# Optimization experiments

Measured on AMD Instinct MI355X. Metric: run time of the kernel, lower is better.

The kernel has to match this reference:

```python
import jax, jax.numpy as jnp
import numpy as np

B, H, W, C = 4, 224, 224, 256
HEADS = 8
WIN = 7
N = WIN * WIN  # 49 tokens per window
MLP_HID = 4 * C
EPS = 1e-5


def _rel_index(w):
    coords = np.stack(np.meshgrid(np.arange(w), np.arange(w), indexing='ij'))  # (2,w,w)
    cf = coords.reshape(2, -1)                       # (2, w*w)
    rc = cf[:, :, None] - cf[:, None, :]             # (2, N, N)
    rc = rc.transpose(1, 2, 0).astype(np.int64)      # (N, N, 2)
    rc[:, :, 0] += w - 1
    rc[:, :, 1] += w - 1
    rc[:, :, 0] *= 2 * w - 1
    return jnp.asarray(rc.sum(-1), dtype=jnp.int32)  # (N, N)


def setup_inputs() -> dict:
    key = jax.random.key(0)
    ks = jax.random.split(key, 6)
    std = 0.02
    return {
        'x': jax.random.normal(ks[0], (B, H, W, C), dtype=jnp.float32),
        'norm1_g': jnp.ones((C,), jnp.float32),
        'norm1_b': jnp.zeros((C,), jnp.float32),
        'qkv_w': jax.random.normal(ks[1], (3 * C, C), jnp.float32) * std,
        'qkv_b': jnp.zeros((3 * C,), jnp.float32),
        'bias_table': jax.random.normal(ks[2], ((2 * WIN - 1) ** 2, HEADS), jnp.float32) * std,
        'proj_w': jax.random.normal(ks[3], (C, C), jnp.float32) * std,
        'proj_b': jnp.zeros((C,), jnp.float32),
        'norm2_g': jnp.ones((C,), jnp.float32),
        'norm2_b': jnp.zeros((C,), jnp.float32),
        'fc1_w': jax.random.normal(ks[4], (MLP_HID, C), jnp.float32) * std,
        'fc1_b': jnp.zeros((MLP_HID,), jnp.float32),
        'fc2_w': jax.random.normal(ks[5], (C, MLP_HID), jnp.float32) * std,
        'fc2_b': jnp.zeros((C,), jnp.float32),
        'rel_index': _rel_index(WIN),
    }


def _layernorm(x, g, b):
    mu = jnp.mean(x, axis=-1, keepdims=True)
    var = jnp.mean(jnp.square(x - mu), axis=-1, keepdims=True)
    return (x - mu) * jax.lax.rsqrt(var + EPS) * g + b


def reference(x, norm1_g, norm1_b, qkv_w, qkv_b, bias_table, proj_w, proj_b,
              norm2_g, norm2_b, fc1_w, fc1_b, fc2_w, fc2_b, rel_index):
    Bc, Hc, Wc, Cc = x.shape
    d = Cc // HEADS
    scale = d ** -0.5
    nh, nw = Hc // WIN, Wc // WIN

    shortcut = x
    h = _layernorm(x, norm1_g, norm1_b)

    # window_partition: (B,H,W,C) -> (B*nW, N, C)
    wins = h.reshape(Bc, nh, WIN, nw, WIN, Cc).transpose(0, 1, 3, 2, 4, 5)
    wins = wins.reshape(-1, N, Cc)

    # qkv projection and split into heads
    qkv = wins @ qkv_w.T + qkv_b                                  # (Bw, N, 3C)
    qkv = qkv.reshape(-1, N, 3, HEADS, d).transpose(2, 0, 3, 1, 4)  # (3, Bw, h, N, d)
    q, k, v = qkv[0], qkv[1], qkv[2]

    attn = jnp.einsum('bhnd,bhmd->bhnm', q, k) * scale            # (Bw, h, N, N)
    bias = bias_table[rel_index.reshape(-1)].reshape(N, N, HEADS).transpose(2, 0, 1)
    attn = jax.nn.softmax(attn + bias[None], axis=-1)

    o = jnp.einsum('bhnm,bhmd->bhnd', attn, v)                    # (Bw, h, N, d)
    o = o.transpose(0, 2, 1, 3).reshape(-1, N, Cc)
    o = o @ proj_w.T + proj_b

    # window_reverse: (B*nW, N, C) -> (B,H,W,C)
    o = o.reshape(Bc, nh, nw, WIN, WIN, Cc).transpose(0, 1, 3, 2, 4, 5)
    o = o.reshape(Bc, Hc, Wc, Cc)

    x = shortcut + o
    h2 = _layernorm(x, norm2_g, norm2_b)
    m = jax.nn.gelu(h2 @ fc1_w.T + fc1_b, approximate=False) @ fc2_w.T + fc2_b
    return x + m
```

## Files before the change

### kernel.cpp

```cpp
#include <hip/hip_runtime.h>

typedef unsigned short u16;
typedef __bf16 bf16x8 __attribute__((ext_vector_type(8)));
typedef float f32x4 __attribute__((ext_vector_type(4)));

#define TOKENS 200704
#define QK_ELEMS 51380224UL

__device__ __forceinline__ u16 f2b(float f) {
    __bf16 h = (__bf16)f;
    return __builtin_bit_cast(u16, h);
}

#define GLDS(g, l) __builtin_amdgcn_global_load_lds( \
    (const __attribute__((address_space(1))) void*)(g), \
    (__attribute__((address_space(3))) void*)(l), 16, 0, 0)

#define MFMA __builtin_amdgcn_mfma_f32_16x16x32_bf16

template<int EPI>
__global__ __launch_bounds__(512, 2)
void gemm256(const u16* __restrict__ A, const u16* __restrict__ W,
             const float* __restrict__ bias, int nt, int K, long moff,
             u16* __restrict__ outb, float* __restrict__ outf,
             const float* __restrict__ res,
             const float* __restrict__ g2, const float* __restrict__ b2,
             u16* __restrict__ h2o)
{
    __shared__ u16 As[2][256 * 64];
    __shared__ u16 Bs[2][256 * 64];
    const int tid  = threadIdx.x;
    const int wave = tid >> 6, lane = tid & 63;

    const int nwg = gridDim.x, bidO = blockIdx.x;
    const int qq = nwg >> 3, rr = nwg & 7;
    const int xcd = bidO & 7, idxx = bidO >> 3;
    const int bid = (xcd < rr) ? (xcd * (qq + 1) + idxx)
                               : (rr * (qq + 1) + (xcd - rr) * qq + idxx);

    const int bm = bid / nt, bn = bid % nt;
    const long m0 = (long)bm * 256;
    const int  n0 = bn * 256;
    const int wr = wave >> 2, wc = wave & 3;
    const int lr = lane & 15, lg = lane >> 4;
    const int crow   = lane >> 3;
    const int ccol_s = ((lane & 7) ^ crow) * 8;
    const int swz    = (lr & 7) * 8;

    f32x4 acc[8][4] = {};

    auto stage = [&](int buf, int k0) {
#pragma unroll
        for (int p = 0; p < 4; ++p) {
            const int i = p * 8 + wave;
            const int row = i * 8 + crow;
            GLDS(A + (m0 + row) * (long)K + k0 + ccol_s, &As[buf][i * 512]);
            GLDS(W + (long)(n0 + row) * K + k0 + ccol_s, &Bs[buf][i * 512]);
        }
    };

    auto compute = [&](int buf) {
        bf16x8 bfr[2][4];
#pragma unroll
        for (int kk2 = 0; kk2 < 2; ++kk2)
#pragma unroll
            for (int fn = 0; fn < 4; ++fn)
                bfr[kk2][fn] = *reinterpret_cast<const bf16x8*>(
                    &Bs[buf][(wc * 64 + fn * 16 + lr) * 64 + ((kk2 * 32 + lg * 8) ^ swz)]);
        bf16x8 aq[2][2], an[2][2];
#pragma unroll
        for (int p = 0; p < 2; ++p)
#pragma unroll
            for (int kk2 = 0; kk2 < 2; ++kk2)
                aq[p][kk2] = *reinterpret_cast<const bf16x8*>(
                    &As[buf][(wr * 128 + p * 16 + lr) * 64 + ((kk2 * 32 + lg * 8) ^ swz)]);
#pragma unroll
        for (int q = 0; q < 4; ++q) {
            bf16x8 (&cur)[2][2] = (q & 1) ? an : aq;
            bf16x8 (&nxt)[2][2] = (q & 1) ? aq : an;
            if (q < 3) {
#pragma unroll
                for (int p = 0; p < 2; ++p)
#pragma unroll
                    for (int kk2 = 0; kk2 < 2; ++kk2)
                        nxt[p][kk2] = *reinterpret_cast<const bf16x8*>(
                            &As[buf][(wr * 128 + (2 * (q + 1) + p) * 16 + lr) * 64 + ((kk2 * 32 + lg * 8) ^ swz)]);
            }
            __builtin_amdgcn_s_setprio(1);
#pragma unroll
            for (int p = 0; p < 2; ++p)
#pragma unroll
                for (int kk2 = 0; kk2 < 2; ++kk2)
#pragma unroll
                    for (int fn = 0; fn < 4; ++fn)
                        acc[2 * q + p][fn] = MFMA(cur[p][kk2], bfr[kk2][fn], acc[2 * q + p][fn], 0, 0, 0);
            __builtin_amdgcn_s_setprio(0);
        }
    };

    const int nk = K >> 6;
    stage(0, 0);
    stage(1, 64);
    int k = 128;
    for (int t = 0; t < nk - 1; ++t) {
        asm volatile("s_waitcnt vmcnt(8)" ::: "memory");
        __builtin_amdgcn_s_barrier();
        __builtin_amdgcn_sched_barrier(0);
        compute(t & 1);
        __builtin_amdgcn_s_barrier();
        __builtin_amdgcn_sched_barrier(0);
        if (t + 2 < nk) {
            stage(t & 1, k); k += 64;
            __builtin_amdgcn_sched_barrier(0);
        }
    }
    asm volatile("s_waitcnt vmcnt(0)" ::: "memory");
    __builtin_amdgcn_s_barrier();
    __builtin_amdgcn_sched_barrier(0);
    compute((nk - 1) & 1);

    if constexpr (EPI == 1) {
        __shared__ float red[2][256][4];
        float g2c[4], b2c[4];
#pragma unroll
        for (int fn = 0; fn < 4; ++fn) {
            const int n = wc * 64 + fn * 16 + lr;
            g2c[fn] = g2[n]; b2c[fn] = b2[n];
        }
#pragma unroll
        for (int fm = 0; fm < 8; ++fm) {
#pragma unroll
            for (int r = 0; r < 4; ++r) {
                const long m = m0 + wr * 128 + fm * 16 + lg * 4 + r;
                float s = 0.f, s2 = 0.f;
#pragma unroll
                for (int fn = 0; fn < 4; ++fn) {
                    const int n = wc * 64 + fn * 16 + lr;
                    const float x2 = acc[fm][fn][r] + bias[n] + res[m * 256 + n];
                    acc[fm][fn][r] = x2;
                    outf[m * 256 + n] = x2;
                    s += x2; s2 += x2 * x2;
                }
#pragma unroll
                for (int d = 1; d < 16; d <<= 1) { s += __shfl_xor(s, d); s2 += __shfl_xor(s2, d); }
                if (lr == 0) {
                    const int tok = wr * 128 + fm * 16 + lg * 4 + r;
                    red[0][tok][wc] = s; red[1][tok][wc] = s2;
                }
            }
        }
        __syncthreads();
#pragma unroll
        for (int fm = 0; fm < 8; ++fm) {
#pragma unroll
            for (int r = 0; r < 4; ++r) {
                const int tok = wr * 128 + fm * 16 + lg * 4 + r;
                const float s  = red[0][tok][0] + red[0][tok][1] + red[0][tok][2] + red[0][tok][3];
                const float q  = red[1][tok][0] + red[1][tok][1] + red[1][tok][2] + red[1][tok][3];
                const float mu = s * 0.00390625f;
                const float rs = rsqrtf(q * 0.00390625f - mu * mu + 1e-5f);
                const long m = m0 + tok;
#pragma unroll
                for (int fn = 0; fn < 4; ++fn) {
                    const int n = wc * 64 + fn * 16 + lr;
                    h2o[m * 256 + n] = f2b((acc[fm][fn][r] - mu) * rs * g2c[fn] + b2c[fn]);
                }
            }
        }
    } else {
#pragma unroll
        for (int fm = 0; fm < 8; ++fm) {
#pragma unroll
            for (int r = 0; r < 4; ++r) {
                const long m = m0 + wr * 128 + fm * 16 + lg * 4 + r;
                size_t mpart = 0;
                if (EPI == 0) {
                    const int gm = (int)(m + moff);
                    const int b = gm / 50176;
                    const int rem = gm % 50176;
                    const int y = rem / 224, x = rem % 224;
                    const int win = (b * 32 + y / 7) * 32 + x / 7;
                    const int pos = (y % 7) * 7 + (x % 7);
                    mpart = (size_t)win * 12544 + (size_t)pos * 32;
                }
#pragma unroll
                for (int fn = 0; fn < 4; ++fn) {
                    const int n = n0 + wc * 64 + fn * 16 + lr;
                    const float v = acc[fm][fn][r];
                    if (EPI == 0) {
                        const int sec = n >> 8, hd = (n >> 5) & 7, d = n & 31;
                        const float sc = (sec == 0) ? 0.17677669529663687f : 1.0f;
                        outb[sec * QK_ELEMS + mpart + hd * 1568 + d] = f2b((v + bias[n]) * sc);
                    } else if (EPI == 2) {
                        const float t = v + bias[n];
                        const float s = t * (1.5957691216f + 0.07135481627f * t * t);
                        const float g = t * __builtin_amdgcn_rcpf(1.0f + __expf(-s));
                        outb[m * 1024 + n] = f2b(g);
                    } else {
                        outf[m * 256 + n] += v + bias[n];
                    }
                }
            }
        }
    }
}

__global__ __launch_bounds__(256)
void layernorm_k(const float* __restrict__ in, const float* __restrict__ g,
                 const float* __restrict__ bb, u16* __restrict__ out)
{
    const int token = blockIdx.x * 4 + (threadIdx.x >> 6);
    const int lane = threadIdx.x & 63;
    const float4 v = *reinterpret_cast<const float4*>(in + (size_t)token * 256 + lane * 4);
    float s  = v.x + v.y + v.z + v.w;
    float s2 = v.x * v.x + v.y * v.y + v.z * v.z + v.w * v.w;
#pragma unroll
    for (int m = 1; m < 64; m <<= 1) { s += __shfl_xor(s, m); s2 += __shfl_xor(s2, m); }
    const float mu  = s * (1.0f / 256.0f);
    const float var = s2 * (1.0f / 256.0f) - mu * mu;
    const float rs  = rsqrtf(var + 1e-5f);
    const float4 gv = *reinterpret_cast<const float4*>(g + lane * 4);
    const float4 bv = *reinterpret_cast<const float4*>(bb + lane * 4);
    ushort4 o;
    o.x = f2b((v.x - mu) * rs * gv.x + bv.x);
    o.y = f2b((v.y - mu) * rs * gv.y + bv.y);
    o.z = f2b((v.z - mu) * rs * gv.z + bv.z);
    o.w = f2b((v.w - mu) * rs * gv.w + bv.w);
    *reinterpret_cast<ushort4*>(out + (size_t)token * 256 + lane * 4) = o;
}

__global__ __launch_bounds__(256)
void attn_win(const u16* __restrict__ qkv, const float* __restrict__ biasF,
              u16* __restrict__ outb, int pair0)
{
    __shared__ u16 plds[4][64 * 72];
    __shared__ u16 vlds[4][32 * 72];
    const int wave = threadIdx.x >> 6, lane = threadIdx.x & 63;
    const int pair = pair0 + blockIdx.x * 4 + wave;
    const int head = pair & 7, win = pair >> 3;
    const int lr = lane & 15, lg = lane >> 4;

    const u16* Q  = qkv + (size_t)pair * 1568;
    const u16* Kp = qkv + QK_ELEMS + (size_t)pair * 1568;
    const u16* Vp = qkv + 2 * QK_ELEMS + (size_t)pair * 1568;

    u16* vl = &vlds[wave][0];
#pragma unroll
    for (int it = 0; it < 8; ++it) {
        const int idx = it * 64 + lane;
        if (idx < 480) vl[(idx / 15) * 72 + 49 + idx % 15] = 0;
    }
#pragma unroll
    for (int it = 0; it < 4; ++it) {
        const int idx = it * 64 + lane;
        if (idx < 196) {
            const int pos = idx >> 2, dc = idx & 3;
            const uint4 vv = *reinterpret_cast<const uint4*>(Vp + pos * 32 + dc * 8);
            u16* dst = vl + (dc * 8) * 72 + pos;
            dst[0 * 72] = (u16)vv.x;  dst[1 * 72] = (u16)(vv.x >> 16);
            dst[2 * 72] = (u16)vv.y;  dst[3 * 72] = (u16)(vv.y >> 16);
            dst[4 * 72] = (u16)vv.z;  dst[5 * 72] = (u16)(vv.z >> 16);
            dst[6 * 72] = (u16)vv.w;  dst[7 * 72] = (u16)(vv.w >> 16);
        }
    }

    bf16x8 qf[4], kf[4];
#pragma unroll
    for (int f = 0; f < 4; ++f) {
        int n = f * 16 + lr; n = n > 48 ? 48 : n;
        qf[f] = *reinterpret_cast<const bf16x8*>(Q  + n * 32 + lg * 8);
        kf[f] = *reinterpret_cast<const bf16x8*>(Kp + n * 32 + lg * 8);
    }
    f32x4 s[4][4] = {};
#pragma unroll
    for (int fm = 0; fm < 4; ++fm)
#pragma unroll
        for (int fn = 0; fn < 4; ++fn)
            s[fm][fn] = MFMA(qf[fm], kf[fn], s[fm][fn], 0, 0, 0);

    const float* bh = biasF + head * 2401;
    u16* pl = &plds[wave][0];
#pragma unroll
    for (int fm = 0; fm < 4; ++fm) {
#pragma unroll
        for (int r = 0; r < 4; ++r) {
            const int row = fm * 16 + lg * 4 + r;
            const int brow = row > 48 ? 48 : row;
            float v[4];
#pragma unroll
            for (int fn = 0; fn < 4; ++fn) {
                const int col = fn * 16 + lr;
                const float bval = bh[brow * 49 + (col > 48 ? 48 : col)];
                v[fn] = (col > 48) ? -3.0e38f : (s[fm][fn][r] + bval);
            }
            float mx = fmaxf(fmaxf(v[0], v[1]), fmaxf(v[2], v[3]));
#pragma unroll
            for (int d = 1; d < 16; d <<= 1) mx = fmaxf(mx, __shfl_xor(mx, d));
            float p[4], sum = 0.f;
#pragma unroll
            for (int fn = 0; fn < 4; ++fn) {
                const int col = fn * 16 + lr;
                p[fn] = (col <= 48) ? __expf(v[fn] - mx) : 0.f;
                sum += p[fn];
            }
#pragma unroll
            for (int d = 1; d < 16; d <<= 1) sum += __shfl_xor(sum, d);
            const float rinv = __builtin_amdgcn_rcpf(sum);
#pragma unroll
            for (int fn = 0; fn < 4; ++fn)
                pl[row * 72 + fn * 16 + lr] = f2b(p[fn] * rinv);
        }
    }
    __syncthreads();

    f32x4 o[4][2] = {};
#pragma unroll
    for (int kc = 0; kc < 2; ++kc) {
        bf16x8 vf[2];
#pragma unroll
        for (int f2 = 0; f2 < 2; ++f2)
            vf[f2] = *reinterpret_cast<const bf16x8*>(vl + (f2 * 16 + lr) * 72 + kc * 32 + lg * 8);
#pragma unroll
        for (int fm = 0; fm < 4; ++fm) {
            const bf16x8 pa = *reinterpret_cast<const bf16x8*>(pl + (fm * 16 + lr) * 72 + kc * 32 + lg * 8);
#pragma unroll
            for (int f2 = 0; f2 < 2; ++f2)
                o[fm][f2] = MFMA(pa, vf[f2], o[fm][f2], 0, 0, 0);
        }
    }

    const int b = win >> 10, rem = win & 1023, wy = rem >> 5, wx = rem & 31;
#pragma unroll
    for (int fm = 0; fm < 4; ++fm) {
#pragma unroll
        for (int r = 0; r < 4; ++r) {
            const int tok = fm * 16 + lg * 4 + r;
            if (tok > 48) continue;
            const int y = wy * 7 + tok / 7, xx = wx * 7 + tok % 7;
            const size_t mrow = ((size_t)(b * 224 + y)) * 224 + xx;
#pragma unroll
            for (int f2 = 0; f2 < 2; ++f2)
                outb[mrow * 256 + head * 32 + f2 * 16 + lr] = f2b(o[fm][f2][r]);
        }
    }
}

__global__ __launch_bounds__(256)
void cvt_w(const float* __restrict__ qw, const float* __restrict__ pw,
           const float* __restrict__ f1, const float* __restrict__ f2,
           u16* __restrict__ outw)
{
    const int t = blockIdx.x * 256 + threadIdx.x;
    float v;
    if (t < 196608) v = qw[t];
    else if (t < 262144) v = pw[t - 196608];
    else if (t < 524288) v = f1[t - 262144];
    else v = f2[t - 524288];
    outw[t] = f2b(v);
}

__global__ __launch_bounds__(256)
void bias_pre(const float* __restrict__ btab, const int* __restrict__ relidx,
              float* __restrict__ biasF)
{
    const int t = blockIdx.x * 256 + threadIdx.x;
    if (t >= 19208) return;
    const int head = t / 2401, ij = t % 2401;
    biasF[t] = btab[relidx[ij] * 8 + head];
}

extern "C" void kernel_launch(void* const* d_in, const int* in_sizes, int n_in,
                              void* d_out, int out_size, void* d_ws, size_t ws_size,
                              hipStream_t stream)
{
    const float* x      = (const float*)d_in[0];
    const float* n1g    = (const float*)d_in[1];
    const float* n1b    = (const float*)d_in[2];
    const float* qkv_w  = (const float*)d_in[3];
    const float* qkv_b  = (const float*)d_in[4];
    const float* btab   = (const float*)d_in[5];
    const float* proj_w = (const float*)d_in[6];
    const float* proj_b = (const float*)d_in[7];
    const float* n2g    = (const float*)d_in[8];
    const float* n2b    = (const float*)d_in[9];
    const float* fc1_w  = (const float*)d_in[10];
    const float* fc1_b  = (const float*)d_in[11];
    const float* fc2_w  = (const float*)d_in[12];
    const float* fc2_b  = (const float*)d_in[13];
    const int*   relidx = (const int*)d_in[14];
    float* out = (float*)d_out;

    char* ws = (char*)d_ws;
    u16*   wbf   = (u16*)ws;
    float* biasF = (float*)(ws + 1572864);
    u16*   hbuf  = (u16*)(ws + 1650688);
    u16*   rbuf  = (u16*)(ws + 1650688 + 102760448);
    const size_t r_avail = ws_size - (1650688 + 102760448);

    const u16* Wq  = wbf;
    const u16* Wp  = wbf + 196608;
    const u16* Wf1 = wbf + 262144;
    const u16* Wf2 = wbf + 524288;

    cvt_w<<<3072, 256, 0, stream>>>(qkv_w, proj_w, fc1_w, fc2_w, wbf);
    bias_pre<<<76, 256, 0, stream>>>(btab, relidx, biasF);
    layernorm_k<<<50176, 256, 0, stream>>>(x, n1g, n1b, hbuf);

    for (int b = 0; b < 4; ++b) {
        gemm256<0><<<588, 512, 0, stream>>>(hbuf + (size_t)b * 50176 * 256, Wq, qkv_b,
                                            3, 256, (long)b * 50176,
                                            rbuf, nullptr, nullptr, nullptr, nullptr, nullptr);
        attn_win<<<2048, 256, 0, stream>>>(rbuf, biasF, hbuf, b * 8192);
    }

    gemm256<1><<<784, 512, 0, stream>>>(hbuf, Wp, proj_b, 1, 256, 0,
                                        nullptr, out, x, n2g, n2b, hbuf);

    long rows_per = 100352;
    if ((long)(r_avail / 2048) < rows_per) rows_per = 50176;
    for (long r0 = 0; r0 < TOKENS; r0 += rows_per) {
        const long rows = (TOKENS - r0 < rows_per) ? (TOKENS - r0) : rows_per;
        gemm256<2><<<(int)((rows / 256) * 4), 512, 0, stream>>>(
            hbuf + r0 * 256, Wf1, fc1_b, 4, 256, 0, rbuf, nullptr, nullptr, nullptr, nullptr, nullptr);
        gemm256<3><<<(int)(rows / 256), 512, 0, stream>>>(
            rbuf, Wf2, fc2_b, 1, 1024, 0, nullptr, out + r0 * 256, nullptr, nullptr, nullptr, nullptr);
    }
}
```

Measured before the change: 1.192 ms.

## Templatize GEMM tile shape, shrink K-step and fuse per-batch QKV/attention launches

Replaces the fixed 256x256 GEMM with a templated kernel that uses 8 waves each holding a 64x64 output tile, with a K-step of 32 and a new LDS swizzle. Tiles become 256x128 for QKV and the MLP and 128x256 for proj, and occupancy targets 4 blocks per CU. The four per-batch QKV GEMM and attention launches are merged into one launch each over all tokens. This needs the rbuf workspace to hold QKV for every batch at once. Smaller tiles give more blocks and better occupancy, but they reuse operands less and double the number of barriers per K.

```diff
diff --git a/kernel.cpp b/kernel.cpp
--- a/kernel.cpp
+++ b/kernel.cpp
@@ -18,17 +18,22 @@
 
 #define MFMA __builtin_amdgcn_mfma_f32_16x16x32_bf16
 
-template<int EPI>
-__global__ __launch_bounds__(512, 2)
-void gemm256(const u16* __restrict__ A, const u16* __restrict__ W,
-             const float* __restrict__ bias, int nt, int K, long moff,
-             u16* __restrict__ outb, float* __restrict__ outf,
-             const float* __restrict__ res,
-             const float* __restrict__ g2, const float* __restrict__ b2,
-             u16* __restrict__ h2o)
-{
-    __shared__ u16 As[2][256 * 64];
-    __shared__ u16 Bs[2][256 * 64];
+template<int EPI, int WR, int WC>
+__global__ __launch_bounds__(512, 4)
+void gemm_t(const u16* __restrict__ A, const u16* __restrict__ W,
+            const float* __restrict__ bias, int nt, int K,
+            u16* __restrict__ outb, float* __restrict__ outf,
+            const float* __restrict__ res,
+            const float* __restrict__ g2, const float* __restrict__ b2,
+            u16* __restrict__ h2o)
+{
+    constexpr int BM = WR * 64, BN = WC * 64;
+    constexpr int ACH = BM / 16;
+    constexpr int TCH = (BM + BN) / 16;
+    __shared__ u16 As[2][BM * 32];
+    __shared__ u16 Bs[2][BN * 32];
+    __shared__ float red[EPI == 1 ? 2 * 128 * 4 : 1];
+
     const int tid  = threadIdx.x;
     const int wave = tid >> 6, lane = tid & 63;
 
@@ -39,88 +44,66 @@
                                : (rr * (qq + 1) + (xcd - rr) * qq + idxx);
 
     const int bm = bid / nt, bn = bid % nt;
-    const long m0 = (long)bm * 256;
-    const int  n0 = bn * 256;
-    const int wr = wave >> 2, wc = wave & 3;
+    const long m0 = (long)bm * BM;
+    const int  n0 = bn * BN;
+    const int wr = wave / WC, wc = wave % WC;
     const int lr = lane & 15, lg = lane >> 4;
-    const int crow   = lane >> 3;
-    const int ccol_s = ((lane & 7) ^ crow) * 8;
-    const int swz    = (lr & 7) * 8;
-
-    f32x4 acc[8][4] = {};
+    const int ccol_s = (((lane & 3) ^ ((lane >> 3) & 3)) * 8);
+    const int swzr = (lg ^ ((lr >> 1) & 3)) * 8;
+
+    f32x4 acc[4][4] = {};
 
     auto stage = [&](int buf, int k0) {
 #pragma unroll
-        for (int p = 0; p < 4; ++p) {
-            const int i = p * 8 + wave;
-            const int row = i * 8 + crow;
-            GLDS(A + (m0 + row) * (long)K + k0 + ccol_s, &As[buf][i * 512]);
-            GLDS(W + (long)(n0 + row) * K + k0 + ccol_s, &Bs[buf][i * 512]);
+        for (int p = 0; p < TCH / 8; ++p) {
+            const int q = p * 8 + wave;
+            const int rq = (q < ACH) ? q : q - ACH;
+            const int row = rq * 16 + (lane >> 2);
+            if (q < ACH)
+                GLDS(A + (m0 + row) * (long)K + k0 + ccol_s, &As[buf][rq * 512]);
+            else
+                GLDS(W + (long)(n0 + row) * K + k0 + ccol_s, &Bs[buf][rq * 512]);
         }
     };
 
     auto compute = [&](int buf) {
-        bf16x8 bfr[2][4];
-#pragma unroll
-        for (int kk2 = 0; kk2 < 2; ++kk2)
+        bf16x8 af[4], bfr[4];
+#pragma unroll
+        for (int fm = 0; fm < 4; ++fm)
+            af[fm] = *reinterpret_cast<const bf16x8*>(
+                &As[buf][(wr * 64 + fm * 16 + lr) * 32 + swzr]);
+#pragma unroll
+        for (int fn = 0; fn < 4; ++fn)
+            bfr[fn] = *reinterpret_cast<const bf16x8*>(
+                &Bs[buf][(wc * 64 + fn * 16 + lr) * 32 + swzr]);
+        __builtin_amdgcn_s_setprio(1);
+#pragma unroll
+        for (int fm = 0; fm < 4; ++fm)
 #pragma unroll
             for (int fn = 0; fn < 4; ++fn)
-                bfr[kk2][fn] = *reinterpret_cast<const bf16x8*>(
-                    &Bs[buf][(wc * 64 + fn * 16 + lr) * 64 + ((kk2 * 32 + lg * 8) ^ swz)]);
-        bf16x8 aq[2][2], an[2][2];
-#pragma unroll
-        for (int p = 0; p < 2; ++p)
-#pragma unroll
-            for (int kk2 = 0; kk2 < 2; ++kk2)
-                aq[p][kk2] = *reinterpret_cast<const bf16x8*>(
-                    &As[buf][(wr * 128 + p * 16 + lr) * 64 + ((kk2 * 32 + lg * 8) ^ swz)]);
-#pragma unroll
-        for (int q = 0; q < 4; ++q) {
-            bf16x8 (&cur)[2][2] = (q & 1) ? an : aq;
-            bf16x8 (&nxt)[2][2] = (q & 1) ? aq : an;
-            if (q < 3) {
-#pragma unroll
-                for (int p = 0; p < 2; ++p)
-#pragma unroll
-                    for (int kk2 = 0; kk2 < 2; ++kk2)
-                        nxt[p][kk2] = *reinterpret_cast<const bf16x8*>(
-                            &As[buf][(wr * 128 + (2 * (q + 1) + p) * 16 + lr) * 64 + ((kk2 * 32 + lg * 8) ^ swz)]);
-            }
-            __builtin_amdgcn_s_setprio(1);
-#pragma unroll
-            for (int p = 0; p < 2; ++p)
-#pragma unroll
-                for (int kk2 = 0; kk2 < 2; ++kk2)
-#pragma unroll
-                    for (int fn = 0; fn < 4; ++fn)
-                        acc[2 * q + p][fn] = MFMA(cur[p][kk2], bfr[kk2][fn], acc[2 * q + p][fn], 0, 0, 0);
-            __builtin_amdgcn_s_setprio(0);
-        }
+                acc[fm][fn] = MFMA(af[fm], bfr[fn], acc[fm][fn], 0, 0, 0);
+        __builtin_amdgcn_s_setprio(0);
     };
 
-    const int nk = K >> 6;
+    const int nk = K >> 5;
     stage(0, 0);
-    stage(1, 64);
-    int k = 128;
-    for (int t = 0; t < nk - 1; ++t) {
-        asm volatile("s_waitcnt vmcnt(8)" ::: "memory");
+    stage(1, 32);
+    int k = 64;
+    for (int t = 0; t < nk; ++t) {
+        if (t == nk - 1) asm volatile("s_waitcnt vmcnt(0)" ::: "memory");
+        else             asm volatile("s_waitcnt vmcnt(3)" ::: "memory");
         __builtin_amdgcn_s_barrier();
         __builtin_amdgcn_sched_barrier(0);
         compute(t & 1);
         __builtin_amdgcn_s_barrier();
         __builtin_amdgcn_sched_barrier(0);
         if (t + 2 < nk) {
-            stage(t & 1, k); k += 64;
+            stage(t & 1, k); k += 32;
             __builtin_amdgcn_sched_barrier(0);
         }
     }
-    asm volatile("s_waitcnt vmcnt(0)" ::: "memory");
-    __builtin_amdgcn_s_barrier();
-    __builtin_amdgcn_sched_barrier(0);
-    compute((nk - 1) & 1);
 
     if constexpr (EPI == 1) {
-        __shared__ float red[2][256][4];
         float g2c[4], b2c[4];
 #pragma unroll
         for (int fn = 0; fn < 4; ++fn) {
@@ -128,10 +111,10 @@
             g2c[fn] = g2[n]; b2c[fn] = b2[n];
         }
 #pragma unroll
-        for (int fm = 0; fm < 8; ++fm) {
+        for (int fm = 0; fm < 4; ++fm) {
 #pragma unroll
             for (int r = 0; r < 4; ++r) {
-                const long m = m0 + wr * 128 + fm * 16 + lg * 4 + r;
+                const long m = m0 + wr * 64 + fm * 16 + lg * 4 + r;
                 float s = 0.f, s2 = 0.f;
 #pragma unroll
                 for (int fn = 0; fn < 4; ++fn) {
@@ -144,19 +127,22 @@
 #pragma unroll
                 for (int d = 1; d < 16; d <<= 1) { s += __shfl_xor(s, d); s2 += __shfl_xor(s2, d); }
                 if (lr == 0) {
-                    const int tok = wr * 128 + fm * 16 + lg * 4 + r;
-                    red[0][tok][wc] = s; red[1][tok][wc] = s2;
+                    const int tok = wr * 64 + fm * 16 + lg * 4 + r;
+                    red[(0 * 128 + tok) * 4 + wc] = s;
+                    red[(1 * 128 + tok) * 4 + wc] = s2;
                 }
             }
         }
         __syncthreads();
 #pragma unroll
-        for (int fm = 0; fm < 8; ++fm) {
+        for (int fm = 0; fm < 4; ++fm) {
 #pragma unroll
             for (int r = 0; r < 4; ++r) {
-                const int tok = wr * 128 + fm * 16 + lg * 4 + r;
-                const float s  = red[0][tok][0] + red[0][tok][1] + red[0][tok][2] + red[0][tok][3];
-                const float q  = red[1][tok][0] + red[1][tok][1] + red[1][tok][2] + red[1][tok][3];
+                const int tok = wr * 64 + fm * 16 + lg * 4 + r;
+                const float s = red[(0 * 128 + tok) * 4 + 0] + red[(0 * 128 + tok) * 4 + 1]
+                              + red[(0 * 128 + tok) * 4 + 2] + red[(0 * 128 + tok) * 4 + 3];
+                const float q = red[(1 * 128 + tok) * 4 + 0] + red[(1 * 128 + tok) * 4 + 1]
+                              + red[(1 * 128 + tok) * 4 + 2] + red[(1 * 128 + tok) * 4 + 3];
                 const float mu = s * 0.00390625f;
                 const float rs = rsqrtf(q * 0.00390625f - mu * mu + 1e-5f);
                 const long m = m0 + tok;
@@ -169,13 +155,13 @@
         }
     } else {
 #pragma unroll
-        for (int fm = 0; fm < 8; ++fm) {
+        for (int fm = 0; fm < 4; ++fm) {
 #pragma unroll
             for (int r = 0; r < 4; ++r) {
-                const long m = m0 + wr * 128 + fm * 16 + lg * 4 + r;
+                const long m = m0 + wr * 64 + fm * 16 + lg * 4 + r;
                 size_t mpart = 0;
                 if (EPI == 0) {
-                    const int gm = (int)(m + moff);
+                    const int gm = (int)m;
                     const int b = gm / 50176;
                     const int rem = gm % 50176;
                     const int y = rem / 224, x = rem % 224;
@@ -231,12 +217,12 @@
 
 __global__ __launch_bounds__(256)
 void attn_win(const u16* __restrict__ qkv, const float* __restrict__ biasF,
-              u16* __restrict__ outb, int pair0)
+              u16* __restrict__ outb)
 {
     __shared__ u16 plds[4][64 * 72];
     __shared__ u16 vlds[4][32 * 72];
     const int wave = threadIdx.x >> 6, lane = threadIdx.x & 63;
-    const int pair = pair0 + blockIdx.x * 4 + wave;
+    const int pair = blockIdx.x * 4 + wave;
     const int head = pair & 7, win = pair >> 3;
     const int lr = lane & 15, lg = lane >> 4;
 
@@ -406,23 +392,20 @@
     bias_pre<<<76, 256, 0, stream>>>(btab, relidx, biasF);
     layernorm_k<<<50176, 256, 0, stream>>>(x, n1g, n1b, hbuf);
 
-    for (int b = 0; b < 4; ++b) {
-        gemm256<0><<<588, 512, 0, stream>>>(hbuf + (size_t)b * 50176 * 256, Wq, qkv_b,
-                                            3, 256, (long)b * 50176,
-                                            rbuf, nullptr, nullptr, nullptr, nullptr, nullptr);
-        attn_win<<<2048, 256, 0, stream>>>(rbuf, biasF, hbuf, b * 8192);
-    }
-
-    gemm256<1><<<784, 512, 0, stream>>>(hbuf, Wp, proj_b, 1, 256, 0,
-                                        nullptr, out, x, n2g, n2b, hbuf);
+    gemm_t<0, 4, 2><<<784 * 6, 512, 0, stream>>>(hbuf, Wq, qkv_b, 6, 256,
+                                                 rbuf, nullptr, nullptr, nullptr, nullptr, nullptr);
+    attn_win<<<8192, 256, 0, stream>>>(rbuf, biasF, hbuf);
+
+    gemm_t<1, 2, 4><<<1568, 512, 0, stream>>>(hbuf, Wp, proj_b, 1, 256,
+                                              nullptr, out, x, n2g, n2b, hbuf);
 
     long rows_per = 100352;
     if ((long)(r_avail / 2048) < rows_per) rows_per = 50176;
     for (long r0 = 0; r0 < TOKENS; r0 += rows_per) {
         const long rows = (TOKENS - r0 < rows_per) ? (TOKENS - r0) : rows_per;
-        gemm256<2><<<(int)((rows / 256) * 4), 512, 0, stream>>>(
-            hbuf + r0 * 256, Wf1, fc1_b, 4, 256, 0, rbuf, nullptr, nullptr, nullptr, nullptr, nullptr);
-        gemm256<3><<<(int)(rows / 256), 512, 0, stream>>>(
-            rbuf, Wf2, fc2_b, 1, 1024, 0, nullptr, out + r0 * 256, nullptr, nullptr, nullptr, nullptr);
-    }
-}
+        gemm_t<2, 4, 2><<<(int)((rows / 256) * 8), 512, 0, stream>>>(
+            hbuf + r0 * 256, Wf1, fc1_b, 8, 256, rbuf, nullptr, nullptr, nullptr, nullptr, nullptr);
+        gemm_t<3, 4, 2><<<(int)((rows / 256) * 2), 512, 0, stream>>>(
+            rbuf, Wf2, fc2_b, 2, 1024, nullptr, out + r0 * 256, nullptr, nullptr, nullptr, nullptr);
+    }
+}
```

Result: faster. 1.108 ms (-7.0%).
